# Kernel tuning notes

Hardware: AMD Instinct MI355X
Metric: run time of the kernel (lower is better)

## Reference

```python
import jax, jax.numpy as jnp
import numpy as np

HEAD_DIM = 64
N_IT = 3
EPS = 1.0  # SinkhornDistance(1, max_iter=n_it)
SCALE = 1.0 / float(np.sqrt(HEAD_DIM))


def setup_inputs() -> dict:
    key = jax.random.key(0)
    kq, kk, kv = jax.random.split(key, 3)
    B, H, S, D = 2, 12, 1024, HEAD_DIM
    q = jax.random.normal(kq, (B, H, S, D), dtype=jnp.float32)
    k = jax.random.normal(kk, (B, H, S, D), dtype=jnp.float32)
    v = jax.random.normal(kv, (B, H, S, D), dtype=jnp.float32)
    attn_mask = jnp.zeros((1, 1, S, S), dtype=bool)  # False -> no position masked
    return {"q": q, "k": k, "v": v, "attn_mask": attn_mask}


def _sinkhorn(scores):
    # Log-domain Sinkhorn-Knopp (sinkformers-style). Cost C = -scores,
    # uniform marginals mu = nu = 1/S, u/v initialized to zero.
    C = -scores                                   # [N, S, S]
    n = C.shape[-2]
    m = C.shape[-1]
    log_mu = -jnp.log(jnp.asarray(n, C.dtype))    # log(1/n)
    log_nu = -jnp.log(jnp.asarray(m, C.dtype))    # log(1/m)

    def M(u, v):
        # modified cost matrix: (-C + u_i + v_j) / eps
        return (-C + u[..., :, None] + v[..., None, :]) / EPS

    def body(carry, _):
        u, v = carry
        u = EPS * (log_mu - jax.scipy.special.logsumexp(M(u, v), axis=-1)) + u
        v = EPS * (log_nu - jax.scipy.special.logsumexp(M(u, v), axis=-2)) + v
        return (u, v), None

    u0 = jnp.zeros(C.shape[:-1], C.dtype)
    v0 = jnp.zeros(C.shape[:-2] + (m,), C.dtype)
    (u, v), _ = jax.lax.scan(body, (u0, v0), None, length=N_IT)
    return jnp.exp(M(u, v))                       # transport plan pi, rows/cols ~ 1/S


def reference(q, k, v, attn_mask):
    B, H, S, D = q.shape
    scores = jnp.einsum('bhqd,bhkd->bhqk', q, k) * SCALE
    scores = jnp.where(attn_mask, jnp.asarray(-1e9, scores.dtype), scores)
    pi = _sinkhorn(scores.reshape(B * H, S, S))
    # pi rows sum to ~1/S; multiply by S so rows sum to ~1 (as in the torch code)
    attn_weights = (pi * S).reshape(B, H, S, S)
    output = jnp.einsum('bhqk,bhkd->bhqd', attn_weights, v)
    return output, attn_weights
```

## Files before the change

### kernel.cpp

```cpp
#include <hip/hip_runtime.h>
#include <hip/hip_fp16.h>
#include <cstddef>
#include <cstdint>


#define NH 24
#define SEQ 1024
#define HD 64
#define NHS (NH * SEQ)

typedef _Float16 f16x8 __attribute__((ext_vector_type(8)));
typedef float f32x4 __attribute__((ext_vector_type(4)));

__global__ __launch_bounds__(256) void k_init(float* __restrict__ z) {
  z[blockIdx.x * 256 + threadIdx.x] = 0.f;
}

template <int MODE>
__global__ __launch_bounds__(256) void k_sweep(const float* __restrict__ q,
                                               const float* __restrict__ kin,
                                               const float* __restrict__ vecPrev,
                                               float* __restrict__ vecOut) {
  __shared__ __align__(16) __half qs[128][72];
  __shared__ __align__(16) __half ks[128][72];
  __shared__ float ws_[128];

  const int bid = blockIdx.x;
  const int swz = (bid & 7) * 192 + (bid >> 3);
  const int h = swz >> 6;
  const int row0 = ((swz >> 3) & 7) << 7;
  const int col0 = (swz & 7) << 7;
  const float* qh = q + (size_t)h * SEQ * HD;
  const float* kh = kin + (size_t)h * SEQ * HD;
  const int t = threadIdx.x;

#pragma unroll
  for (int it = 0; it < 8; ++it) {
    int f = t + (it << 8);
    int r = f >> 4, c4 = (f & 15) << 2;
    float4 v = *(const float4*)(qh + (size_t)(row0 + r) * HD + c4);
    *(__half2*)&qs[r][c4] = __floats2half2_rn(v.x, v.y);
    *(__half2*)&qs[r][c4 + 2] = __floats2half2_rn(v.z, v.w);
    float4 u = *(const float4*)(kh + (size_t)(col0 + r) * HD + c4);
    *(__half2*)&ks[r][c4] = __floats2half2_rn(u.x, u.y);
    *(__half2*)&ks[r][c4 + 2] = __floats2half2_rn(u.z, u.w);
  }
  if (MODE == 1 && t < 128) ws_[t] = (1.0f / 1024.0f) / vecPrev[h * SEQ + col0 + t];
  if (MODE == 2 && t < 128) ws_[t] = (1.0f / 1024.0f) / vecPrev[h * SEQ + row0 + t];
  __syncthreads();

  const int w = t >> 6, lane = t & 63;
  const int ln = lane & 15, ko = lane >> 4;
  const int rb = (w & 1) << 6, cb = (w >> 1) << 6;
  f32x4 acc[4][4] = {};
#pragma unroll
  for (int kk = 0; kk < 2; ++kk) {
    f16x8 af[4], bf[4];
#pragma unroll
    for (int m = 0; m < 4; ++m)
      af[m] = *(const f16x8*)&qs[rb + m * 16 + ln][(kk << 5) + (ko << 3)];
#pragma unroll
    for (int n = 0; n < 4; ++n)
      bf[n] = *(const f16x8*)&ks[cb + n * 16 + ln][(kk << 5) + (ko << 3)];
#pragma unroll
    for (int m = 0; m < 4; ++m)
#pragma unroll
      for (int n = 0; n < 4; ++n)
        acc[m][n] = __builtin_amdgcn_mfma_f32_16x16x32_f16(af[m], bf[n], acc[m][n], 0, 0, 0);
  }

#pragma unroll
  for (int m = 0; m < 4; ++m)
#pragma unroll
    for (int n = 0; n < 4; ++n)
#pragma unroll
      for (int r = 0; r < 4; ++r)
        acc[m][n][r] = __expf(acc[m][n][r] * 0.125f);

  if (MODE == 2) {
    float* cs = vecOut + h * SEQ;
#pragma unroll
    for (int n = 0; n < 4; ++n) {
      float s = 0.f;
#pragma unroll
      for (int m = 0; m < 4; ++m)
#pragma unroll
        for (int r = 0; r < 4; ++r)
          s += acc[m][n][r] * ws_[rb + m * 16 + (ko << 2) + r];
      s += __shfl_xor(s, 16);
      s += __shfl_xor(s, 32);
      if (lane < 16) atomicAdd(&cs[col0 + cb + n * 16 + ln], s);
    }
  } else {
    float* rd = vecOut + h * SEQ;
#pragma unroll
    for (int m = 0; m < 4; ++m)
#pragma unroll
      for (int r = 0; r < 4; ++r) {
        float s;
        if (MODE == 1) {
          s = acc[m][0][r] * ws_[cb + ln] + acc[m][1][r] * ws_[cb + 16 + ln]
            + acc[m][2][r] * ws_[cb + 32 + ln] + acc[m][3][r] * ws_[cb + 48 + ln];
        } else {
          s = acc[m][0][r] + acc[m][1][r] + acc[m][2][r] + acc[m][3][r];
        }
        s += __shfl_xor(s, 1, 16); s += __shfl_xor(s, 2, 16);
        s += __shfl_xor(s, 4, 16); s += __shfl_xor(s, 8, 16);
        if (ln == 0) atomicAdd(&rd[row0 + rb + m * 16 + (ko << 2) + r], s);
      }
  }
}

__global__ __launch_bounds__(256) void k_final(const float* __restrict__ q,
                                               const float* __restrict__ kin,
                                               const float* __restrict__ vin,
                                               const float* __restrict__ rd2,
                                               const float* __restrict__ cs2,
                                               float* __restrict__ attn,
                                               float* __restrict__ out) {
  __shared__ __align__(16) __half qs[32][72];
  __shared__ __align__(16) __half ks[128][72];
  __shared__ __align__(16) __half vt[64][136];
  __shared__ __align__(16) __half ps16[32][136];
  __shared__ float binv[128];
  __shared__ float a_s[32];

  const int bid = blockIdx.x;
  const int swz = (bid & 7) * 96 + (bid >> 3);
  const int h = swz >> 5;
  const int rblk = swz & 31;
  const int grow0 = h * SEQ + (rblk << 5);
  const float* qh = q + (size_t)h * SEQ * HD;
  const float* kh = kin + (size_t)h * SEQ * HD;
  const float* Vh = vin + (size_t)h * SEQ * HD;
  const int t = threadIdx.x;
  const int w = t >> 6, lane = t & 63, ln = lane & 15, ko = lane >> 4;

#pragma unroll
  for (int it = 0; it < 2; ++it) {
    int f = t + (it << 8);
    int r = f >> 4, c4 = (f & 15) << 2;
    float4 v = *(const float4*)(qh + (size_t)((rblk << 5) + r) * HD + c4);
    *(__half2*)&qs[r][c4] = __floats2half2_rn(v.x, v.y);
    *(__half2*)&qs[r][c4 + 2] = __floats2half2_rn(v.z, v.w);
  }
  if (t < 32) a_s[t] = (1.0f / 1024.0f) / rd2[grow0 + t];

  f32x4 acc_o[2] = {};

  for (int c = 0; c < 8; ++c) {
    const int j0 = c << 7;
    __syncthreads();
#pragma unroll
    for (int it = 0; it < 8; ++it) {
      int f = t + (it << 8);
      int j = f >> 4, c4 = (f & 15) << 2;
      float4 u = *(const float4*)(kh + (size_t)(j0 + j) * HD + c4);
      *(__half2*)&ks[j][c4] = __floats2half2_rn(u.x, u.y);
      *(__half2*)&ks[j][c4 + 2] = __floats2half2_rn(u.z, u.w);
    }
#pragma unroll
    for (int it = 0; it < 4; ++it) {
      int c4 = (w << 2) + (it << 4);
      int j = t & 63;
      float4 v0 = *(const float4*)(Vh + (size_t)(j0 + j) * HD + c4);
      vt[c4 + 0][j] = __float2half(v0.x);
      vt[c4 + 1][j] = __float2half(v0.y);
      vt[c4 + 2][j] = __float2half(v0.z);
      vt[c4 + 3][j] = __float2half(v0.w);
      float4 v1 = *(const float4*)(Vh + (size_t)(j0 + 64 + j) * HD + c4);
      vt[c4 + 0][64 + j] = __float2half(v1.x);
      vt[c4 + 1][64 + j] = __float2half(v1.y);
      vt[c4 + 2][64 + j] = __float2half(v1.z);
      vt[c4 + 3][64 + j] = __float2half(v1.w);
    }
    if (t < 128) binv[t] = 1.0f / cs2[h * SEQ + j0 + t];
    __syncthreads();

    const int cw = w << 5;
    f32x4 acc[2][2] = {};
#pragma unroll
    for (int kk = 0; kk < 2; ++kk) {
      f16x8 af[2], bf[2];
#pragma unroll
      for (int m = 0; m < 2; ++m)
        af[m] = *(const f16x8*)&qs[m * 16 + ln][(kk << 5) + (ko << 3)];
#pragma unroll
      for (int n = 0; n < 2; ++n)
        bf[n] = *(const f16x8*)&ks[cw + n * 16 + ln][(kk << 5) + (ko << 3)];
#pragma unroll
      for (int m = 0; m < 2; ++m)
#pragma unroll
        for (int n = 0; n < 2; ++n)
          acc[m][n] = __builtin_amdgcn_mfma_f32_16x16x32_f16(af[m], bf[n], acc[m][n], 0, 0, 0);
    }
#pragma unroll
    for (int m = 0; m < 2; ++m)
#pragma unroll
      for (int n = 0; n < 2; ++n)
#pragma unroll
        for (int r = 0; r < 4; ++r) {
          int row = m * 16 + (ko << 2) + r;
          int col = cw + n * 16 + ln;
          float av = __expf(acc[m][n][r] * 0.125f) * a_s[row] * binv[col];
          ps16[row][col] = __float2half(av);
        }
    __syncthreads();

    {
      int row = t >> 3, cg = (t & 7) << 4;
      f16x8 h0 = *(const f16x8*)&ps16[row][cg];
      f16x8 h1 = *(const f16x8*)&ps16[row][cg + 8];
      float* ap = attn + (size_t)(grow0 + row) * SEQ + j0 + cg;
      float4 o0 = make_float4((float)h0[0], (float)h0[1], (float)h0[2], (float)h0[3]);
      float4 o1 = make_float4((float)h0[4], (float)h0[5], (float)h0[6], (float)h0[7]);
      float4 o2 = make_float4((float)h1[0], (float)h1[1], (float)h1[2], (float)h1[3]);
      float4 o3 = make_float4((float)h1[4], (float)h1[5], (float)h1[6], (float)h1[7]);
      *(float4*)ap = o0; *(float4*)(ap + 4) = o1;
      *(float4*)(ap + 8) = o2; *(float4*)(ap + 12) = o3;
    }
#pragma unroll
    for (int ks_ = 0; ks_ < 4; ++ks_) {
      f16x8 a = *(const f16x8*)&ps16[((w & 1) << 4) + ln][(ks_ << 5) + (ko << 3)];
#pragma unroll
      for (int dt = 0; dt < 2; ++dt) {
        f16x8 b = *(const f16x8*)&vt[((w >> 1) << 5) + dt * 16 + ln][(ks_ << 5) + (ko << 3)];
        acc_o[dt] = __builtin_amdgcn_mfma_f32_16x16x32_f16(a, b, acc_o[dt], 0, 0, 0);
      }
    }
  }

#pragma unroll
  for (int dt = 0; dt < 2; ++dt)
#pragma unroll
    for (int r = 0; r < 4; ++r) {
      int row = grow0 + ((w & 1) << 4) + (ko << 2) + r;
      int d = ((w >> 1) << 5) + dt * 16 + ln;
      out[(size_t)row * HD + d] = acc_o[dt][r];
    }
}

extern "C" void kernel_launch(void* const* d_in, const int* in_sizes, int n_in,
                              void* d_out, int out_size, void* d_ws, size_t ws_size,
                              hipStream_t stream) {
  const float* q = (const float*)d_in[0];
  const float* k = (const float*)d_in[1];
  const float* v = (const float*)d_in[2];
  (void)in_sizes; (void)n_in; (void)out_size; (void)ws_size;

  float* out = (float*)d_out;
  float* attn = out + (size_t)NH * SEQ * HD;

  float* wsf = (float*)d_ws;
  float* rd0 = wsf;
  float* cs0 = wsf + 1 * NHS;
  float* rd1 = wsf + 2 * NHS;
  float* cs1 = wsf + 3 * NHS;
  float* rd2 = wsf + 4 * NHS;
  float* cs2 = wsf + 5 * NHS;

  k_init<<<6 * NHS / 256, 256, 0, stream>>>(wsf);
  k_sweep<0><<<1536, 256, 0, stream>>>(q, k, rd0, rd0);
  k_sweep<2><<<1536, 256, 0, stream>>>(q, k, rd0, cs0);
  k_sweep<1><<<1536, 256, 0, stream>>>(q, k, cs0, rd1);
  k_sweep<2><<<1536, 256, 0, stream>>>(q, k, rd1, cs1);
  k_sweep<1><<<1536, 256, 0, stream>>>(q, k, cs1, rd2);
  k_sweep<2><<<1536, 256, 0, stream>>>(q, k, rd2, cs2);
  k_final<<<768, 256, 0, stream>>>(q, k, v, rd2, cs2, attn, out);
}
```

Measured before the change: 138.3 us.

## Precast Q/K/V to fp16 once and read MFMA operands directly from global

A new prep kernel converts Q and K to fp16 and V to a transposed fp16 layout once, and zeroes the workspace in the same launch. The sweep and final kernels then load MFMA fragments straight from these fp16 buffers instead of staging fp32 data through shared memory. The final kernel is also retiled to 16-row blocks with all column scalings cached in LDS, and it writes attn with nontemporal stores. This halves the bytes read for Q/K in every sweep and removes LDS staging and syncs, at the cost of an extra prep pass and uncached, non-coalesced-by-LDS fragment loads from global/L2.

```diff
diff --git a/kernel.cpp b/kernel.cpp
--- a/kernel.cpp
+++ b/kernel.cpp
@@ -12,56 +12,83 @@
 typedef _Float16 f16x8 __attribute__((ext_vector_type(8)));
 typedef float f32x4 __attribute__((ext_vector_type(4)));
 
-__global__ __launch_bounds__(256) void k_init(float* __restrict__ z) {
-  z[blockIdx.x * 256 + threadIdx.x] = 0.f;
+__global__ __launch_bounds__(256) void k_prep(const float* __restrict__ q,
+                                              const float* __restrict__ kin,
+                                              const float* __restrict__ v,
+                                              __half* __restrict__ q16,
+                                              __half* __restrict__ k16,
+                                              __half* __restrict__ vt16,
+                                              float* __restrict__ zvec) {
+  const int b = blockIdx.x;
+  const int z = b / 768;
+  const int bb = b - z * 768;
+  const int t = threadIdx.x;
+  if (z < 2) {
+    const float* src = z ? kin : q;
+    __half* dst = z ? k16 : q16;
+    size_t u = ((size_t)bb * 256 + t) * 8;
+    const float4* s4 = (const float4*)(src + u);
+    float4 a = s4[0], c = s4[1];
+    f16x8 h;
+    h[0] = (_Float16)a.x; h[1] = (_Float16)a.y; h[2] = (_Float16)a.z; h[3] = (_Float16)a.w;
+    h[4] = (_Float16)c.x; h[5] = (_Float16)c.y; h[6] = (_Float16)c.z; h[7] = (_Float16)c.w;
+    *(f16x8*)(dst + u) = h;
+    if (z == 0) {
+      int gid = bb * 256 + t;
+      if (gid < 6 * NHS) zvec[gid] = 0.f;
+    }
+  } else {
+    __shared__ float ld[64][33];
+    const int h = bb >> 5, s0 = (bb & 31) << 5;
+    const float* Vh = v + (size_t)h * SEQ * HD;
+#pragma unroll
+    for (int it = 0; it < 2; ++it) {
+      int f = t + (it << 8);
+      int r = f >> 4, c4 = (f & 15) << 2;
+      float4 vv = *(const float4*)(Vh + (size_t)(s0 + r) * HD + c4);
+      ld[c4 + 0][r] = vv.x; ld[c4 + 1][r] = vv.y;
+      ld[c4 + 2][r] = vv.z; ld[c4 + 3][r] = vv.w;
+    }
+    __syncthreads();
+    int d = t >> 2, sg = (t & 3) << 3;
+    f16x8 h8;
+#pragma unroll
+    for (int i = 0; i < 8; ++i) h8[i] = (_Float16)ld[d][sg + i];
+    *(f16x8*)(vt16 + (size_t)h * HD * SEQ + (size_t)d * SEQ + s0 + sg) = h8;
+  }
 }
 
 template <int MODE>
-__global__ __launch_bounds__(256) void k_sweep(const float* __restrict__ q,
-                                               const float* __restrict__ kin,
+__global__ __launch_bounds__(256) void k_sweep(const __half* __restrict__ q16,
+                                               const __half* __restrict__ k16,
                                                const float* __restrict__ vecPrev,
                                                float* __restrict__ vecOut) {
-  __shared__ __align__(16) __half qs[128][72];
-  __shared__ __align__(16) __half ks[128][72];
   __shared__ float ws_[128];
-
   const int bid = blockIdx.x;
   const int swz = (bid & 7) * 192 + (bid >> 3);
   const int h = swz >> 6;
   const int row0 = ((swz >> 3) & 7) << 7;
   const int col0 = (swz & 7) << 7;
-  const float* qh = q + (size_t)h * SEQ * HD;
-  const float* kh = kin + (size_t)h * SEQ * HD;
   const int t = threadIdx.x;
-
-#pragma unroll
-  for (int it = 0; it < 8; ++it) {
-    int f = t + (it << 8);
-    int r = f >> 4, c4 = (f & 15) << 2;
-    float4 v = *(const float4*)(qh + (size_t)(row0 + r) * HD + c4);
-    *(__half2*)&qs[r][c4] = __floats2half2_rn(v.x, v.y);
-    *(__half2*)&qs[r][c4 + 2] = __floats2half2_rn(v.z, v.w);
-    float4 u = *(const float4*)(kh + (size_t)(col0 + r) * HD + c4);
-    *(__half2*)&ks[r][c4] = __floats2half2_rn(u.x, u.y);
-    *(__half2*)&ks[r][c4 + 2] = __floats2half2_rn(u.z, u.w);
-  }
   if (MODE == 1 && t < 128) ws_[t] = (1.0f / 1024.0f) / vecPrev[h * SEQ + col0 + t];
   if (MODE == 2 && t < 128) ws_[t] = (1.0f / 1024.0f) / vecPrev[h * SEQ + row0 + t];
-  __syncthreads();
+  if (MODE) __syncthreads();
 
   const int w = t >> 6, lane = t & 63;
   const int ln = lane & 15, ko = lane >> 4;
   const int rb = (w & 1) << 6, cb = (w >> 1) << 6;
+  const __half* qh = q16 + ((size_t)h << 16);
+  const __half* kh = k16 + ((size_t)h << 16);
   f32x4 acc[4][4] = {};
 #pragma unroll
   for (int kk = 0; kk < 2; ++kk) {
     f16x8 af[4], bf[4];
 #pragma unroll
     for (int m = 0; m < 4; ++m)
-      af[m] = *(const f16x8*)&qs[rb + m * 16 + ln][(kk << 5) + (ko << 3)];
+      af[m] = *(const f16x8*)(qh + (size_t)(row0 + rb + m * 16 + ln) * HD + kk * 32 + ko * 8);
 #pragma unroll
     for (int n = 0; n < 4; ++n)
-      bf[n] = *(const f16x8*)&ks[cb + n * 16 + ln][(kk << 5) + (ko << 3)];
+      bf[n] = *(const f16x8*)(kh + (size_t)(col0 + cb + n * 16 + ln) * HD + kk * 32 + ko * 8);
 #pragma unroll
     for (int m = 0; m < 4; ++m)
 #pragma unroll
@@ -111,133 +138,85 @@
   }
 }
 
-__global__ __launch_bounds__(256) void k_final(const float* __restrict__ q,
-                                               const float* __restrict__ kin,
-                                               const float* __restrict__ vin,
+__global__ __launch_bounds__(256) void k_final(const __half* __restrict__ q16,
+                                               const __half* __restrict__ k16,
+                                               const __half* __restrict__ vt16,
                                                const float* __restrict__ rd2,
                                                const float* __restrict__ cs2,
                                                float* __restrict__ attn,
                                                float* __restrict__ out) {
-  __shared__ __align__(16) __half qs[32][72];
-  __shared__ __align__(16) __half ks[128][72];
-  __shared__ __align__(16) __half vt[64][136];
-  __shared__ __align__(16) __half ps16[32][136];
-  __shared__ float binv[128];
-  __shared__ float a_s[32];
-
+  __shared__ __align__(16) __half ps16[16][136];
+  __shared__ float binv[1024];
+  __shared__ float a_s[16];
   const int bid = blockIdx.x;
-  const int swz = (bid & 7) * 96 + (bid >> 3);
-  const int h = swz >> 5;
-  const int rblk = swz & 31;
-  const int grow0 = h * SEQ + (rblk << 5);
-  const float* qh = q + (size_t)h * SEQ * HD;
-  const float* kh = kin + (size_t)h * SEQ * HD;
-  const float* Vh = vin + (size_t)h * SEQ * HD;
+  const int swz = (bid & 7) * 192 + (bid >> 3);
+  const int h = swz >> 6;
+  const int rblk = swz & 63;
   const int t = threadIdx.x;
   const int w = t >> 6, lane = t & 63, ln = lane & 15, ko = lane >> 4;
 
 #pragma unroll
-  for (int it = 0; it < 2; ++it) {
-    int f = t + (it << 8);
-    int r = f >> 4, c4 = (f & 15) << 2;
-    float4 v = *(const float4*)(qh + (size_t)((rblk << 5) + r) * HD + c4);
-    *(__half2*)&qs[r][c4] = __floats2half2_rn(v.x, v.y);
-    *(__half2*)&qs[r][c4 + 2] = __floats2half2_rn(v.z, v.w);
-  }
-  if (t < 32) a_s[t] = (1.0f / 1024.0f) / rd2[grow0 + t];
-
-  f32x4 acc_o[2] = {};
+  for (int i = 0; i < 4; ++i) {
+    int idx = t + (i << 8);
+    binv[idx] = 1.0f / cs2[h * SEQ + idx];
+  }
+  if (t < 16) a_s[t] = (1.0f / 1024.0f) / rd2[h * SEQ + rblk * 16 + t];
+
+  const __half* qh = q16 + ((size_t)h << 16);
+  const __half* kh = k16 + ((size_t)h << 16);
+  const __half* vth = vt16 + ((size_t)h << 16);
+  f16x8 aq[2];
+#pragma unroll
+  for (int kk = 0; kk < 2; ++kk)
+    aq[kk] = *(const f16x8*)(qh + (size_t)(rblk * 16 + ln) * HD + kk * 32 + ko * 8);
+
+  const int cw = w << 5;
+  const int dw = w << 4;
+  f32x4 acc_o = {};
+  __syncthreads();
 
   for (int c = 0; c < 8; ++c) {
     const int j0 = c << 7;
+    f32x4 sacc[2] = {};
+#pragma unroll
+    for (int kk = 0; kk < 2; ++kk) {
+#pragma unroll
+      for (int n = 0; n < 2; ++n) {
+        f16x8 bf = *(const f16x8*)(kh + (size_t)(j0 + cw + n * 16 + ln) * HD + kk * 32 + ko * 8);
+        sacc[n] = __builtin_amdgcn_mfma_f32_16x16x32_f16(aq[kk], bf, sacc[n], 0, 0, 0);
+      }
+    }
+#pragma unroll
+    for (int n = 0; n < 2; ++n)
+#pragma unroll
+      for (int r = 0; r < 4; ++r) {
+        int row = (ko << 2) + r;
+        int col = cw + n * 16 + ln;
+        ps16[row][col] = __float2half(__expf(sacc[n][r] * 0.125f) * a_s[row] * binv[j0 + col]);
+      }
     __syncthreads();
-#pragma unroll
-    for (int it = 0; it < 8; ++it) {
-      int f = t + (it << 8);
-      int j = f >> 4, c4 = (f & 15) << 2;
-      float4 u = *(const float4*)(kh + (size_t)(j0 + j) * HD + c4);
-      *(__half2*)&ks[j][c4] = __floats2half2_rn(u.x, u.y);
-      *(__half2*)&ks[j][c4 + 2] = __floats2half2_rn(u.z, u.w);
-    }
-#pragma unroll
-    for (int it = 0; it < 4; ++it) {
-      int c4 = (w << 2) + (it << 4);
-      int j = t & 63;
-      float4 v0 = *(const float4*)(Vh + (size_t)(j0 + j) * HD + c4);
-      vt[c4 + 0][j] = __float2half(v0.x);
-      vt[c4 + 1][j] = __float2half(v0.y);
-      vt[c4 + 2][j] = __float2half(v0.z);
-      vt[c4 + 3][j] = __float2half(v0.w);
-      float4 v1 = *(const float4*)(Vh + (size_t)(j0 + 64 + j) * HD + c4);
-      vt[c4 + 0][64 + j] = __float2half(v1.x);
-      vt[c4 + 1][64 + j] = __float2half(v1.y);
-      vt[c4 + 2][64 + j] = __float2half(v1.z);
-      vt[c4 + 3][64 + j] = __float2half(v1.w);
-    }
-    if (t < 128) binv[t] = 1.0f / cs2[h * SEQ + j0 + t];
+    {
+      int arow = t >> 4, cg = (t & 15) << 3;
+      f16x8 hv = *(const f16x8*)&ps16[arow][cg];
+      f32x4 o0, o1;
+#pragma unroll
+      for (int i = 0; i < 4; ++i) { o0[i] = (float)hv[i]; o1[i] = (float)hv[4 + i]; }
+      float* ap = attn + (size_t)(h * SEQ + rblk * 16 + arow) * SEQ + j0 + cg;
+      __builtin_nontemporal_store(o0, (f32x4*)ap);
+      __builtin_nontemporal_store(o1, (f32x4*)(ap + 4));
+    }
+#pragma unroll
+    for (int ks = 0; ks < 4; ++ks) {
+      f16x8 pa = *(const f16x8*)&ps16[ln][ks * 32 + ko * 8];
+      f16x8 bv = *(const f16x8*)(vth + (size_t)(dw + ln) * SEQ + j0 + ks * 32 + ko * 8);
+      acc_o = __builtin_amdgcn_mfma_f32_16x16x32_f16(pa, bv, acc_o, 0, 0, 0);
+    }
     __syncthreads();
-
-    const int cw = w << 5;
-    f32x4 acc[2][2] = {};
-#pragma unroll
-    for (int kk = 0; kk < 2; ++kk) {
-      f16x8 af[2], bf[2];
-#pragma unroll
-      for (int m = 0; m < 2; ++m)
-        af[m] = *(const f16x8*)&qs[m * 16 + ln][(kk << 5) + (ko << 3)];
-#pragma unroll
-      for (int n = 0; n < 2; ++n)
-        bf[n] = *(const f16x8*)&ks[cw + n * 16 + ln][(kk << 5) + (ko << 3)];
-#pragma unroll
-      for (int m = 0; m < 2; ++m)
-#pragma unroll
-        for (int n = 0; n < 2; ++n)
-          acc[m][n] = __builtin_amdgcn_mfma_f32_16x16x32_f16(af[m], bf[n], acc[m][n], 0, 0, 0);
-    }
-#pragma unroll
-    for (int m = 0; m < 2; ++m)
-#pragma unroll
-      for (int n = 0; n < 2; ++n)
-#pragma unroll
-        for (int r = 0; r < 4; ++r) {
-          int row = m * 16 + (ko << 2) + r;
-          int col = cw + n * 16 + ln;
-          float av = __expf(acc[m][n][r] * 0.125f) * a_s[row] * binv[col];
-          ps16[row][col] = __float2half(av);
-        }
-    __syncthreads();
-
-    {
-      int row = t >> 3, cg = (t & 7) << 4;
-      f16x8 h0 = *(const f16x8*)&ps16[row][cg];
-      f16x8 h1 = *(const f16x8*)&ps16[row][cg + 8];
-      float* ap = attn + (size_t)(grow0 + row) * SEQ + j0 + cg;
-      float4 o0 = make_float4((float)h0[0], (float)h0[1], (float)h0[2], (float)h0[3]);
-      float4 o1 = make_float4((float)h0[4], (float)h0[5], (float)h0[6], (float)h0[7]);
-      float4 o2 = make_float4((float)h1[0], (float)h1[1], (float)h1[2], (float)h1[3]);
-      float4 o3 = make_float4((float)h1[4], (float)h1[5], (float)h1[6], (float)h1[7]);
-      *(float4*)ap = o0; *(float4*)(ap + 4) = o1;
-      *(float4*)(ap + 8) = o2; *(float4*)(ap + 12) = o3;
-    }
-#pragma unroll
-    for (int ks_ = 0; ks_ < 4; ++ks_) {
-      f16x8 a = *(const f16x8*)&ps16[((w & 1) << 4) + ln][(ks_ << 5) + (ko << 3)];
-#pragma unroll
-      for (int dt = 0; dt < 2; ++dt) {
-        f16x8 b = *(const f16x8*)&vt[((w >> 1) << 5) + dt * 16 + ln][(ks_ << 5) + (ko << 3)];
-        acc_o[dt] = __builtin_amdgcn_mfma_f32_16x16x32_f16(a, b, acc_o[dt], 0, 0, 0);
-      }
-    }
-  }
-
-#pragma unroll
-  for (int dt = 0; dt < 2; ++dt)
-#pragma unroll
-    for (int r = 0; r < 4; ++r) {
-      int row = grow0 + ((w & 1) << 4) + (ko << 2) + r;
-      int d = ((w >> 1) << 5) + dt * 16 + ln;
-      out[(size_t)row * HD + d] = acc_o[dt][r];
-    }
+  }
+
+#pragma unroll
+  for (int r = 0; r < 4; ++r)
+    out[(size_t)(h * SEQ + rblk * 16 + (ko << 2) + r) * HD + dw + ln] = acc_o[r];
 }
 
 extern "C" void kernel_launch(void* const* d_in, const int* in_sizes, int n_in,
@@ -258,13 +237,16 @@
   float* cs1 = wsf + 3 * NHS;
   float* rd2 = wsf + 4 * NHS;
   float* cs2 = wsf + 5 * NHS;
-
-  k_init<<<6 * NHS / 256, 256, 0, stream>>>(wsf);
-  k_sweep<0><<<1536, 256, 0, stream>>>(q, k, rd0, rd0);
-  k_sweep<2><<<1536, 256, 0, stream>>>(q, k, rd0, cs0);
-  k_sweep<1><<<1536, 256, 0, stream>>>(q, k, cs0, rd1);
-  k_sweep<2><<<1536, 256, 0, stream>>>(q, k, rd1, cs1);
-  k_sweep<1><<<1536, 256, 0, stream>>>(q, k, cs1, rd2);
-  k_sweep<2><<<1536, 256, 0, stream>>>(q, k, rd2, cs2);
-  k_final<<<768, 256, 0, stream>>>(q, k, v, rd2, cs2, attn, out);
-}
+  __half* q16 = (__half*)(wsf + 6 * NHS);
+  __half* k16 = q16 + (size_t)NH * SEQ * HD;
+  __half* vt16 = k16 + (size_t)NH * SEQ * HD;
+
+  k_prep<<<2304, 256, 0, stream>>>(q, k, v, q16, k16, vt16, wsf);
+  k_sweep<0><<<1536, 256, 0, stream>>>(q16, k16, rd0, rd0);
+  k_sweep<2><<<1536, 256, 0, stream>>>(q16, k16, rd0, cs0);
+  k_sweep<1><<<1536, 256, 0, stream>>>(q16, k16, cs0, rd1);
+  k_sweep<2><<<1536, 256, 0, stream>>>(q16, k16, rd1, cs1);
+  k_sweep<1><<<1536, 256, 0, stream>>>(q16, k16, cs1, rd2);
+  k_sweep<2><<<1536, 256, 0, stream>>>(q16, k16, rd2, cs2);
+  k_final<<<1536, 256, 0, stream>>>(q16, k16, vt16, rd2, cs2, attn, out);
+}
```

After: 168.8 us. 22.1% more time.
